# Kernel optimization log

Measured on AMD Instinct MI355X. Metric: run time of the kernel, lower is better.

Reference implementation:

```python
import jax, jax.numpy as jnp
import numpy as np


def setup_inputs() -> dict:
    key = jax.random.key(0)
    k1, k2 = jax.random.split(key)
    B, C, H, W = 64, 2, 512, 512
    inp = jax.random.normal(k1, (B, C, H, W), dtype=jnp.float32)
    tgt = jax.random.uniform(k2, (B, C, H, W), dtype=jnp.float32)
    return {"input": inp, "target": tgt}


def reference(input, target):
    B, C, H, W = input.shape
    # coordinate maps: x_map[:, j] = (j+1)/W, y_map[p, :] = (p+1)/H
    x_map = (jnp.arange(W, dtype=input.dtype) + 1.0) / W  # (W,)
    y_map = (jnp.arange(H, dtype=input.dtype) + 1.0) / H  # (H,)

    # DSNT soft-argmax: softmax over flattened H*W per (batch, keypoint)
    p = jax.nn.softmax(input.reshape(B, C, H * W), axis=-1).reshape(B, C, H, W)
    pred_x = jnp.einsum('bchw,w->bc', p, x_map)  # normalized coords
    pred_y = jnp.einsum('bchw,h->bc', p, y_map)

    # ground truth via flat argmax (matches torch.argmax on the 2D map)
    am = jnp.argmax(target.reshape(B, C, H * W), axis=-1)  # (B, C) int
    true_x = ((am % W) + 1).astype(input.dtype) / W
    true_y = ((am // W) + 1).astype(input.dtype) / H

    # convert normalized coords to pixel coords
    pred_xp, pred_yp = pred_x * W, pred_y * H
    true_xp, true_yp = true_x * W, true_y * H

    x_diff = true_xp - pred_xp  # (B, C)
    y_diff = true_yp - pred_yp

    s_x = jnp.sum(jnp.sqrt(x_diff ** 2)).reshape(1)
    s_y = jnp.sum(jnp.sqrt(y_diff ** 2)).reshape(1)

    ed = jnp.sqrt(x_diff ** 2 + y_diff ** 2)  # (B, C) per-point pixel ED
    s_i = jnp.sum(ed[:, 0]).reshape(1)          # keypoint o == 0
    s_s = jnp.sum(ed[:, 1:]).reshape(1)         # keypoints o > 0
    tot_list = jnp.sum(ed, axis=1)              # (B,)

    # diameter: distance between keypoint 0 and keypoint 1
    vpx, vpy = pred_xp[:, 0] - pred_xp[:, 1], pred_yp[:, 0] - pred_yp[:, 1]
    vtx, vty = true_xp[:, 0] - true_xp[:, 1], true_yp[:, 0] - true_yp[:, 1]
    pred_dist = jnp.sqrt(vpx ** 2 + vpy ** 2)
    true_dist = jnp.sqrt(vtx ** 2 + vty ** 2)
    diam_list = jnp.sqrt((pred_dist - true_dist) ** 2)  # (B,)
    s_diam = jnp.sum(diam_list).reshape(1)

    return (s_i, s_s, s_i + s_s, s_diam, tot_list, diam_list, s_x, s_y, B)
```

## Files before the change

### kernel.cpp

```cpp
#include <hip/hip_runtime.h>
#include <math.h>
#include <float.h>


namespace {
constexpr int S_SPLIT = 16;
constexpr int PAIRS   = 128;
constexpr int HW      = 512 * 512;
constexpr int CHUNK4  = HW / 4 / S_SPLIT;

typedef float f4 __attribute__((ext_vector_type(4)));

struct Partial {
    float l, sx, sy, tval;
    int   tidx;
    int   pad0, pad1, pad2;
};
}

__global__ __launch_bounds__(256, 4) void dsnt_partial(
        const float* __restrict__ inp,
        const float* __restrict__ tgt,
        Partial* __restrict__ part) {
    const int blk   = blockIdx.x;
    const int pair  = blk >> 4;
    const int split = blk & (S_SPLIT - 1);
    const int tid   = threadIdx.x;
    const f4* in4 = reinterpret_cast<const f4*>(inp + (size_t)pair * HW) + split * CHUNK4;
    const f4* tg4 = reinterpret_cast<const f4*>(tgt + (size_t)pair * HW) + split * CHUNK4;
    const int base4 = split * CHUNK4;
    const float inv = 1.0f / 512.0f;

    const int w0 = (tid * 4) & 511;
    const float fx0 = (float)(w0 + 1) * inv;
    const float fx1 = (float)(w0 + 2) * inv;
    const float fx2 = (float)(w0 + 3) * inv;
    const float fx3 = (float)(w0 + 4) * inv;
    const int rowbase0 = split * 32 + (tid >> 7);

    float l = 0.f, sx = 0.f, sy = 0.f;
    float tv = -1.0f;
    int   ti = 0;

    auto acc = [&](f4 x, f4 t, float fy, int idx) {
        const float e0 = __expf(x.x);
        const float e1 = __expf(x.y);
        const float e2 = __expf(x.z);
        const float e3 = __expf(x.w);
        const float es = (e0 + e1) + (e2 + e3);
        l += es;
        sy = fmaf(es, fy, sy);
        sx = fmaf(e0, fx0, fmaf(e1, fx1, fmaf(e2, fx2, fmaf(e3, fx3, sx))));
        bool g;
        g = t.x > tv; tv = g ? t.x : tv; ti = g ? idx     : ti;
        g = t.y > tv; tv = g ? t.y : tv; ti = g ? idx + 1 : ti;
        g = t.z > tv; tv = g ? t.z : tv; ti = g ? idx + 2 : ti;
        g = t.w > tv; tv = g ? t.w : tv; ti = g ? idx + 3 : ti;
    };

    #pragma unroll
    for (int s = 0; s < 4; ++s) {
        const int i0 = tid + s * 1024;
        const f4 x0 = __builtin_nontemporal_load(&in4[i0]);
        const f4 x1 = __builtin_nontemporal_load(&in4[i0 + 256]);
        const f4 x2 = __builtin_nontemporal_load(&in4[i0 + 512]);
        const f4 x3 = __builtin_nontemporal_load(&in4[i0 + 768]);
        const f4 t0 = __builtin_nontemporal_load(&tg4[i0]);
        const f4 t1 = __builtin_nontemporal_load(&tg4[i0 + 256]);
        const f4 t2 = __builtin_nontemporal_load(&tg4[i0 + 512]);
        const f4 t3 = __builtin_nontemporal_load(&tg4[i0 + 768]);

        const int rb = rowbase0 + 8 * s;
        acc(x0, t0, (float)(rb + 1) * inv, (base4 + i0) * 4);
        acc(x1, t1, (float)(rb + 3) * inv, (base4 + i0 + 256) * 4);
        acc(x2, t2, (float)(rb + 5) * inv, (base4 + i0 + 512) * 4);
        acc(x3, t3, (float)(rb + 7) * inv, (base4 + i0 + 768) * 4);
    }

    for (int off = 32; off > 0; off >>= 1) {
        l  += __shfl_down(l,  off);
        sx += __shfl_down(sx, off);
        sy += __shfl_down(sy, off);
        const float ov = __shfl_down(tv, off);
        const int   oi = __shfl_down(ti, off);
        if (ov > tv || (ov == tv && oi < ti)) { tv = ov; ti = oi; }
    }

    __shared__ float sl[4], ssx[4], ssy[4], stv[4];
    __shared__ int   sti[4];
    const int wid  = tid >> 6;
    const int lane = tid & 63;
    if (lane == 0) { sl[wid] = l; ssx[wid] = sx; ssy[wid] = sy; stv[wid] = tv; sti[wid] = ti; }
    __syncthreads();

    if (tid == 0) {
        float L = 0.f, SX = 0.f, SY = 0.f, TV = -1.0f;
        int TI = 0x7fffffff;
        #pragma unroll
        for (int w = 0; w < 4; ++w) {
            L += sl[w]; SX += ssx[w]; SY += ssy[w];
            if (stv[w] > TV || (stv[w] == TV && sti[w] < TI)) { TV = stv[w]; TI = sti[w]; }
        }
        Partial p;
        p.l = L; p.sx = SX; p.sy = SY; p.tval = TV; p.tidx = TI;
        p.pad0 = p.pad1 = p.pad2 = 0;
        part[blk] = p;
    }
}

__global__ __launch_bounds__(1024) void dsnt_final(
        const Partial* __restrict__ part,
        float* __restrict__ out, int out_size) {
    __shared__ float pxp[PAIRS], pyp[PAIRS], txp[PAIRS], typ[PAIRS];
    __shared__ float edl[PAIRS], axl[PAIRS], ayl[PAIRS];
    const int tid = threadIdx.x;

    const Partial a = part[2 * tid];
    const Partial b = part[2 * tid + 1];
    float L = a.l + b.l, SX = a.sx + b.sx, SY = a.sy + b.sy;
    float tv = a.tval; int ti = a.tidx;
    if (b.tval > tv || (b.tval == tv && b.tidx < ti)) { tv = b.tval; ti = b.tidx; }

    #pragma unroll
    for (int off = 1; off < 8; off <<= 1) {
        L  += __shfl_xor(L,  off);
        SX += __shfl_xor(SX, off);
        SY += __shfl_xor(SY, off);
        const float ov = __shfl_xor(tv, off);
        const int   oi = __shfl_xor(ti, off);
        if (ov > tv || (ov == tv && oi < ti)) { tv = ov; ti = oi; }
    }

    if ((tid & 7) == 0) {
        const int p = tid >> 3;
        const float px = SX / L * 512.0f;
        const float py = SY / L * 512.0f;
        const float tx = (float)((ti & 511) + 1);
        const float ty = (float)((ti >> 9) + 1);
        const float xd = tx - px, yd = ty - py;
        pxp[p] = px; pyp[p] = py; txp[p] = tx; typ[p] = ty;
        edl[p] = sqrtf(xd * xd + yd * yd);
        axl[p] = fabsf(xd);
        ayl[p] = fabsf(yd);
    }
    __syncthreads();

    if (tid < 64) {
        const int bb = tid;
        const float e0 = edl[2 * bb], e1 = edl[2 * bb + 1];
        out[4 + bb] = e0 + e1;
        const float vpx = pxp[2 * bb] - pxp[2 * bb + 1], vpy = pyp[2 * bb] - pyp[2 * bb + 1];
        const float vtx = txp[2 * bb] - txp[2 * bb + 1], vty = typ[2 * bb] - typ[2 * bb + 1];
        const float pd = sqrtf(vpx * vpx + vpy * vpy);
        const float td = sqrtf(vtx * vtx + vty * vty);
        const float diam = fabsf(pd - td);
        out[68 + bb] = diam;

        float si = e0, ss = e1, sd = diam;
        float sxs = axl[2 * bb] + axl[2 * bb + 1];
        float sys = ayl[2 * bb] + ayl[2 * bb + 1];
        #pragma unroll
        for (int off = 32; off > 0; off >>= 1) {
            si  += __shfl_xor(si,  off);
            ss  += __shfl_xor(ss,  off);
            sd  += __shfl_xor(sd,  off);
            sxs += __shfl_xor(sxs, off);
            sys += __shfl_xor(sys, off);
        }
        if (tid == 0) {
            out[0] = si;
            out[1] = ss;
            out[2] = si + ss;
            out[3] = sd;
            out[132] = sxs;
            out[133] = sys;
            if (out_size >= 135) out[134] = 64.0f;
        }
    }
}

extern "C" void kernel_launch(void* const* d_in, const int* in_sizes, int n_in,
                              void* d_out, int out_size, void* d_ws, size_t ws_size,
                              hipStream_t stream) {
    const float* inp = (const float*)d_in[0];
    const float* tgt = (const float*)d_in[1];
    float* out = (float*)d_out;
    Partial* part = (Partial*)d_ws;

    dsnt_partial<<<PAIRS * S_SPLIT, 256, 0, stream>>>(inp, tgt, part);
    dsnt_final<<<1, 1024, 0, stream>>>(part, out, out_size);
}
```

Measured before the change: 251.0 us.

## Split softmax and argmax into separate block sets reading one tensor each

Doubles the grid so the first half of the blocks handles the softmax-weighted coordinate sums over the input and the second half handles the argmax over the target. Each block issues all 16 of its vector loads up front into registers before computing. The partial results move to two separate workspace arrays that the final kernel combines. The aim is more blocks in flight and more loads outstanding per thread to hide memory latency. The cost is extra block launches and branch divergence at the block level.

```diff
diff --git a/kernel.cpp b/kernel.cpp
--- a/kernel.cpp
+++ b/kernel.cpp
@@ -8,118 +8,128 @@
 constexpr int PAIRS   = 128;
 constexpr int HW      = 512 * 512;
 constexpr int CHUNK4  = HW / 4 / S_SPLIT;
+constexpr int SBLK    = PAIRS * S_SPLIT;
+constexpr int NBLK    = 2 * SBLK;
 
 typedef float f4 __attribute__((ext_vector_type(4)));
 
-struct Partial {
-    float l, sx, sy, tval;
-    int   tidx;
-    int   pad0, pad1, pad2;
-};
-}
+struct SoftPart { float l, sx, sy, pad; };
+struct ArgPart  { float tval; int tidx; };
+}
+
+#define NTL(p) __builtin_nontemporal_load(p)
 
 __global__ __launch_bounds__(256, 4) void dsnt_partial(
         const float* __restrict__ inp,
         const float* __restrict__ tgt,
-        Partial* __restrict__ part) {
-    const int blk   = blockIdx.x;
-    const int pair  = blk >> 4;
-    const int split = blk & (S_SPLIT - 1);
-    const int tid   = threadIdx.x;
-    const f4* in4 = reinterpret_cast<const f4*>(inp + (size_t)pair * HW) + split * CHUNK4;
-    const f4* tg4 = reinterpret_cast<const f4*>(tgt + (size_t)pair * HW) + split * CHUNK4;
-    const int base4 = split * CHUNK4;
+        SoftPart* __restrict__ spart,
+        ArgPart* __restrict__ apart) {
+    const int blk = blockIdx.x;
+    const int tid = threadIdx.x;
+    const bool is_soft = blk < SBLK;
+    const int sub   = is_soft ? blk : blk - SBLK;
+    const int pair  = sub >> 4;
+    const int split = sub & (S_SPLIT - 1);
+    const float* base = (is_soft ? inp : tgt) + (size_t)pair * HW;
+    const f4* src = reinterpret_cast<const f4*>(base) + split * CHUNK4;
     const float inv = 1.0f / 512.0f;
 
-    const int w0 = (tid * 4) & 511;
-    const float fx0 = (float)(w0 + 1) * inv;
-    const float fx1 = (float)(w0 + 2) * inv;
-    const float fx2 = (float)(w0 + 3) * inv;
-    const float fx3 = (float)(w0 + 4) * inv;
-    const int rowbase0 = split * 32 + (tid >> 7);
-
-    float l = 0.f, sx = 0.f, sy = 0.f;
-    float tv = -1.0f;
-    int   ti = 0;
-
-    auto acc = [&](f4 x, f4 t, float fy, int idx) {
-        const float e0 = __expf(x.x);
-        const float e1 = __expf(x.y);
-        const float e2 = __expf(x.z);
-        const float e3 = __expf(x.w);
-        const float es = (e0 + e1) + (e2 + e3);
-        l += es;
-        sy = fmaf(es, fy, sy);
-        sx = fmaf(e0, fx0, fmaf(e1, fx1, fmaf(e2, fx2, fmaf(e3, fx3, sx))));
-        bool g;
-        g = t.x > tv; tv = g ? t.x : tv; ti = g ? idx     : ti;
-        g = t.y > tv; tv = g ? t.y : tv; ti = g ? idx + 1 : ti;
-        g = t.z > tv; tv = g ? t.z : tv; ti = g ? idx + 2 : ti;
-        g = t.w > tv; tv = g ? t.w : tv; ti = g ? idx + 3 : ti;
-    };
-
+    f4 v[16];
     #pragma unroll
-    for (int s = 0; s < 4; ++s) {
-        const int i0 = tid + s * 1024;
-        const f4 x0 = __builtin_nontemporal_load(&in4[i0]);
-        const f4 x1 = __builtin_nontemporal_load(&in4[i0 + 256]);
-        const f4 x2 = __builtin_nontemporal_load(&in4[i0 + 512]);
-        const f4 x3 = __builtin_nontemporal_load(&in4[i0 + 768]);
-        const f4 t0 = __builtin_nontemporal_load(&tg4[i0]);
-        const f4 t1 = __builtin_nontemporal_load(&tg4[i0 + 256]);
-        const f4 t2 = __builtin_nontemporal_load(&tg4[i0 + 512]);
-        const f4 t3 = __builtin_nontemporal_load(&tg4[i0 + 768]);
-
-        const int rb = rowbase0 + 8 * s;
-        acc(x0, t0, (float)(rb + 1) * inv, (base4 + i0) * 4);
-        acc(x1, t1, (float)(rb + 3) * inv, (base4 + i0 + 256) * 4);
-        acc(x2, t2, (float)(rb + 5) * inv, (base4 + i0 + 512) * 4);
-        acc(x3, t3, (float)(rb + 7) * inv, (base4 + i0 + 768) * 4);
-    }
-
-    for (int off = 32; off > 0; off >>= 1) {
-        l  += __shfl_down(l,  off);
-        sx += __shfl_down(sx, off);
-        sy += __shfl_down(sy, off);
-        const float ov = __shfl_down(tv, off);
-        const int   oi = __shfl_down(ti, off);
-        if (ov > tv || (ov == tv && oi < ti)) { tv = ov; ti = oi; }
-    }
-
-    __shared__ float sl[4], ssx[4], ssy[4], stv[4];
-    __shared__ int   sti[4];
+    for (int k = 0; k < 16; ++k) v[k] = NTL(&src[tid + k * 256]);
+
+    __shared__ float s0[4], s1[4], s2[4];
+    __shared__ int   s3[4];
     const int wid  = tid >> 6;
     const int lane = tid & 63;
-    if (lane == 0) { sl[wid] = l; ssx[wid] = sx; ssy[wid] = sy; stv[wid] = tv; sti[wid] = ti; }
-    __syncthreads();
-
-    if (tid == 0) {
-        float L = 0.f, SX = 0.f, SY = 0.f, TV = -1.0f;
-        int TI = 0x7fffffff;
+
+    if (is_soft) {
+        const int w0 = (tid * 4) & 511;
+        const float fx0 = (float)(w0 + 1) * inv;
+        const float fx1 = (float)(w0 + 2) * inv;
+        const float fx2 = (float)(w0 + 3) * inv;
+        const float fx3 = (float)(w0 + 4) * inv;
+        const int rb = split * 32 + (tid >> 7);
+
+        float l = 0.f, sx = 0.f, sy = 0.f;
         #pragma unroll
-        for (int w = 0; w < 4; ++w) {
-            L += sl[w]; SX += ssx[w]; SY += ssy[w];
-            if (stv[w] > TV || (stv[w] == TV && sti[w] < TI)) { TV = stv[w]; TI = sti[w]; }
-        }
-        Partial p;
-        p.l = L; p.sx = SX; p.sy = SY; p.tval = TV; p.tidx = TI;
-        p.pad0 = p.pad1 = p.pad2 = 0;
-        part[blk] = p;
+        for (int k = 0; k < 16; ++k) {
+            const f4 x = v[k];
+            const float fy = (float)(rb + 2 * k + 1) * inv;
+            const float e0 = __expf(x.x);
+            const float e1 = __expf(x.y);
+            const float e2 = __expf(x.z);
+            const float e3 = __expf(x.w);
+            const float es = (e0 + e1) + (e2 + e3);
+            l += es;
+            sy = fmaf(es, fy, sy);
+            sx = fmaf(e0, fx0, fmaf(e1, fx1, fmaf(e2, fx2, fmaf(e3, fx3, sx))));
+        }
+        for (int off = 32; off > 0; off >>= 1) {
+            l  += __shfl_down(l,  off);
+            sx += __shfl_down(sx, off);
+            sy += __shfl_down(sy, off);
+        }
+        if (lane == 0) { s0[wid] = l; s1[wid] = sx; s2[wid] = sy; }
+        __syncthreads();
+        if (tid == 0) {
+            SoftPart p;
+            p.l  = (s0[0] + s0[1]) + (s0[2] + s0[3]);
+            p.sx = (s1[0] + s1[1]) + (s1[2] + s1[3]);
+            p.sy = (s2[0] + s2[1]) + (s2[2] + s2[3]);
+            p.pad = 0.f;
+            spart[sub] = p;
+        }
+    } else {
+        const int base4 = split * CHUNK4;
+        float tv = -1.0f;
+        int   ti = 0;
+        #pragma unroll
+        for (int k = 0; k < 16; ++k) {
+            const f4 t = v[k];
+            const int idx = (base4 + tid + k * 256) * 4;
+            bool g;
+            g = t.x > tv; tv = g ? t.x : tv; ti = g ? idx     : ti;
+            g = t.y > tv; tv = g ? t.y : tv; ti = g ? idx + 1 : ti;
+            g = t.z > tv; tv = g ? t.z : tv; ti = g ? idx + 2 : ti;
+            g = t.w > tv; tv = g ? t.w : tv; ti = g ? idx + 3 : ti;
+        }
+        for (int off = 32; off > 0; off >>= 1) {
+            const float ov = __shfl_down(tv, off);
+            const int   oi = __shfl_down(ti, off);
+            if (ov > tv || (ov == tv && oi < ti)) { tv = ov; ti = oi; }
+        }
+        if (lane == 0) { s0[wid] = tv; s3[wid] = ti; }
+        __syncthreads();
+        if (tid == 0) {
+            float TV = -1.0f; int TI = 0x7fffffff;
+            #pragma unroll
+            for (int w = 0; w < 4; ++w)
+                if (s0[w] > TV || (s0[w] == TV && s3[w] < TI)) { TV = s0[w]; TI = s3[w]; }
+            ArgPart p; p.tval = TV; p.tidx = TI;
+            apart[sub] = p;
+        }
     }
 }
 
 __global__ __launch_bounds__(1024) void dsnt_final(
-        const Partial* __restrict__ part,
+        const SoftPart* __restrict__ spart,
+        const ArgPart* __restrict__ apart,
         float* __restrict__ out, int out_size) {
     __shared__ float pxp[PAIRS], pyp[PAIRS], txp[PAIRS], typ[PAIRS];
     __shared__ float edl[PAIRS], axl[PAIRS], ayl[PAIRS];
     const int tid = threadIdx.x;
-
-    const Partial a = part[2 * tid];
-    const Partial b = part[2 * tid + 1];
+    const int g = tid >> 3;
+    const int j = tid & 7;
+
+    const SoftPart a = spart[g * 16 + 2 * j];
+    const SoftPart b = spart[g * 16 + 2 * j + 1];
     float L = a.l + b.l, SX = a.sx + b.sx, SY = a.sy + b.sy;
-    float tv = a.tval; int ti = a.tidx;
-    if (b.tval > tv || (b.tval == tv && b.tidx < ti)) { tv = b.tval; ti = b.tidx; }
+
+    const ArgPart c = apart[g * 16 + 2 * j];
+    const ArgPart d = apart[g * 16 + 2 * j + 1];
+    float tv = c.tval; int ti = c.tidx;
+    if (d.tval > tv || (d.tval == tv && d.tidx < ti)) { tv = d.tval; ti = d.tidx; }
 
     #pragma unroll
     for (int off = 1; off < 8; off <<= 1) {
@@ -131,17 +141,16 @@
         if (ov > tv || (ov == tv && oi < ti)) { tv = ov; ti = oi; }
     }
 
-    if ((tid & 7) == 0) {
-        const int p = tid >> 3;
+    if (j == 0) {
         const float px = SX / L * 512.0f;
         const float py = SY / L * 512.0f;
         const float tx = (float)((ti & 511) + 1);
         const float ty = (float)((ti >> 9) + 1);
         const float xd = tx - px, yd = ty - py;
-        pxp[p] = px; pyp[p] = py; txp[p] = tx; typ[p] = ty;
-        edl[p] = sqrtf(xd * xd + yd * yd);
-        axl[p] = fabsf(xd);
-        ayl[p] = fabsf(yd);
+        pxp[g] = px; pyp[g] = py; txp[g] = tx; typ[g] = ty;
+        edl[g] = sqrtf(xd * xd + yd * yd);
+        axl[g] = fabsf(xd);
+        ayl[g] = fabsf(yd);
     }
     __syncthreads();
 
@@ -185,8 +194,9 @@
     const float* inp = (const float*)d_in[0];
     const float* tgt = (const float*)d_in[1];
     float* out = (float*)d_out;
-    Partial* part = (Partial*)d_ws;
-
-    dsnt_partial<<<PAIRS * S_SPLIT, 256, 0, stream>>>(inp, tgt, part);
-    dsnt_final<<<1, 1024, 0, stream>>>(part, out, out_size);
-}
+    SoftPart* spart = (SoftPart*)d_ws;
+    ArgPart*  apart = (ArgPart*)((char*)d_ws + SBLK * sizeof(SoftPart));
+
+    dsnt_partial<<<NBLK, 256, 0, stream>>>(inp, tgt, spart, apart);
+    dsnt_final<<<1, 1024, 0, stream>>>(spart, apart, out, out_size);
+}
```

Result: slower. 256.2 us (median of 2 runs) (+2.1%).
